# Kernel tuning notes

Hardware: AMD Instinct MI355X
Metric: run time of the kernel (lower is better)

The kernel has to match this reference:

```python
import jax, jax.numpy as jnp
import numpy as np

EMSIZE = 2048
NCLASS = 128
D1 = 2
D2 = 2
NSENT = 32768


def setup_inputs() -> dict:
    key = jax.random.key(0)
    k1, k2, k3 = jax.random.split(key, 3)
    x = jax.random.normal(k1, (NSENT, 1, EMSIZE), dtype=jnp.float32)
    # Scaled-normal params (original uses nn.init.normal_; scaling keeps tanh unsaturated)
    W1 = jax.random.normal(k2, (D1 + 1, EMSIZE, NCLASS), dtype=jnp.float32) / np.float32(np.sqrt(EMSIZE))
    b1 = jnp.zeros((1, NCLASS), dtype=jnp.float32)
    W2 = jax.random.normal(k3, (D2 + 1, NCLASS, NCLASS), dtype=jnp.float32) / np.float32(np.sqrt(NCLASS))
    b2 = jnp.zeros((1, NCLASS), dtype=jnp.float32)
    return {"structural_representations": x, "W1": W1, "b1": b1, "W2": W2, "b2": b2}


def _shift_down(y, k, n):
    # y[p] -> y[p-k], zeros for p < k (causal shift along sentence axis)
    return jnp.pad(y, ((k, 0), (0, 0)))[:n] if k > 0 else y


def reference(structural_representations, W1, b1, W2, b2):
    x = structural_representations  # [N, 1, E]
    n, _, e = x.shape
    d1 = W1.shape[0] - 1
    d2 = W2.shape[0] - 1
    c = W1.shape[-1]
    xs = x.reshape(n, e)  # [N, E]

    # Stage 1: S[p] = sum_{k=0..d1, k<=p} (x[p-k] @ W1[k] + b1)
    Y = jnp.einsum('ne,kec->knc', xs, W1)  # [d1+1, N, C]: one big GEMM per tap
    S = sum(_shift_down(Y[k], k, n) for k in range(d1 + 1))  # windowed causal sum
    pos = jnp.arange(n)
    cnt1 = (jnp.minimum(pos, d1) + 1).astype(xs.dtype)  # bias added once per valid tap
    H = jnp.tanh(S + cnt1[:, None] * b1[0])  # [N, C]

    # Stage 2 (i >= d2): Z[i] = sum_{j=0..d2} H[i-d2+j] @ W2[j] + (d2+1)*b2
    G = jnp.einsum('nc,kcd->knd', H, W2)  # [d2+1, N, C]
    Z = sum(_shift_down(G[j], d2 - j, n) for j in range(d2 + 1)) + (d2 + 1) * b2[0]

    # Fallback for i < d2: single term tanh(x[i]@W1[0]+b1) @ W2[0] + b2
    H0 = jnp.tanh(xs @ W1[0] + b1[0])
    Z0 = H0 @ W2[0] + b2[0]
    Z = jnp.where((pos >= d2)[:, None], Z, Z0)

    out = jax.nn.log_softmax(Z, axis=-1)
    return out.reshape(n, 1, c)
```

## Files before the change

### kernel.cpp

```cpp
#include <hip/hip_runtime.h>
#include <math.h>

typedef __attribute__((ext_vector_type(8))) short short8;
typedef __attribute__((ext_vector_type(4))) float f32x4;

#define MFMA16(a, b, c) __builtin_amdgcn_mfma_f32_16x16x32_bf16((a), (b), (c), 0, 0, 0)

__device__ inline void gl_lds16(const void* g, void* l) {
  __builtin_amdgcn_global_load_lds(
      (const __attribute__((address_space(1))) void*)g,
      (__attribute__((address_space(3))) void*)l, 16, 0, 0);
}

__device__ inline unsigned int pack2(float lo, float hi) {
  unsigned int ulo = __float_as_uint(lo), uhi = __float_as_uint(hi);
  return (uhi & 0xFFFF0000u) | (ulo >> 16);
}
__device__ inline unsigned short f2bf_r(float f) {
  return (unsigned short)((__float_as_uint(f) + 0x8000u) >> 16);
}
__device__ inline float bf2f(unsigned short h) {
  return __uint_as_float(((unsigned int)h) << 16);
}

__global__ __launch_bounds__(256) void k_repack_w1(const float* __restrict__ W1,
                                                   unsigned short* __restrict__ W1bt) {
  __shared__ float tile[64 * 128];
  const int b = blockIdx.x;
  const int k = b >> 5, et = b & 31;
  const int e0 = et * 64;
  const int tid = threadIdx.x;
  const float* src = W1 + (size_t)k * 262144 + (size_t)e0 * 128;
#pragma unroll
  for (int i = 0; i < 8; ++i) {
    int idx4 = tid + i * 256;
    ((f32x4*)tile)[idx4] = ((const f32x4*)src)[idx4];
  }
  __syncthreads();
#pragma unroll
  for (int i = 0; i < 4; ++i) {
    int item = tid + i * 256;
    int c = item >> 3, eo = (item & 7) * 8;
    union { unsigned short h[8]; uint4 v; } t;
#pragma unroll
    for (int u = 0; u < 8; ++u) t.h[u] = f2bf_r(tile[(eo + u) * 128 + c]);
    *(uint4*)(W1bt + (size_t)(k * 128 + c) * 2048 + e0 + eo) = t.v;
  }
}

__global__ __launch_bounds__(256) void k_repack_w2(const float* __restrict__ W2,
                                                   unsigned short* __restrict__ W2t) {
  int idx = blockIdx.x * 256 + threadIdx.x;
  int j = idx >> 14, r = idx & 16383, d = r >> 7, c = r & 127;
  W2t[idx] = f2bf_r(W2[(size_t)j * 16384 + (size_t)c * 128 + d]);
}

__global__ __launch_bounds__(256, 3) void k_gemm1(const float* __restrict__ X,
                                                  const unsigned short* __restrict__ Bt,
                                                  float* __restrict__ Y) {
  __shared__ float Alds[128 * 64];
  __shared__ unsigned short Blds[128 * 64];

  const int g = blockIdx.x;
  const int grp = g / 24, within = g % 24;
  const int cb = within >> 3, rb = grp * 8 + (within & 7);
  const int row0 = rb * 128, col0 = cb * 128;

  const int tid = threadIdx.x, wave = tid >> 6, lane = tid & 63;
  const int mrow = lane & 15, quad = lane >> 4;

  const float* agp[8];
#pragma unroll
  for (int r = 0; r < 8; ++r) {
    int row = wave * 32 + r * 4 + (lane >> 4);
    int c = (lane & 15) ^ (row & 15);
    agp[r] = X + (size_t)(row0 + row) * 2048 + c * 4;
  }
  const unsigned short* bgp[4];
#pragma unroll
  for (int r = 0; r < 4; ++r) {
    int col = wave * 32 + r * 8 + (lane >> 3);
    int c = (lane & 7) ^ (col & 7);
    bgp[r] = Bt + (size_t)(col0 + col) * 2048 + c * 8;
  }

  const int wr = (wave >> 1) * 64, wc = (wave & 1) * 64;

  f32x4 acc[4][4] = {};

  for (int k0 = 0; k0 < 2048; k0 += 64) {
#pragma unroll
    for (int r = 0; r < 8; ++r)
      gl_lds16(agp[r], (char*)Alds + (wave * 32 + r * 4) * 256);
#pragma unroll
    for (int r = 0; r < 4; ++r)
      gl_lds16(bgp[r], (char*)Blds + (wave * 32 + r * 8) * 128);
#pragma unroll
    for (int r = 0; r < 8; ++r) agp[r] += 64;
#pragma unroll
    for (int r = 0; r < 4; ++r) bgp[r] += 64;
    __syncthreads();

#pragma unroll
    for (int s = 0; s < 2; ++s) {
      short8 af[4];
#pragma unroll
      for (int rt = 0; rt < 4; ++rt) {
        int row = wr + rt * 16 + mrow;
        int c0 = s * 8 + quad * 2;
        const float* base = Alds + row * 64;
        f32x4 x0 = *(const f32x4*)(base + ((c0 ^ (row & 15)) * 4));
        f32x4 x1 = *(const f32x4*)(base + (((c0 + 1) ^ (row & 15)) * 4));
        union { unsigned int u[4]; short8 v; } t;
        t.u[0] = pack2(x0[0], x0[1]); t.u[1] = pack2(x0[2], x0[3]);
        t.u[2] = pack2(x1[0], x1[1]); t.u[3] = pack2(x1[2], x1[3]);
        af[rt] = t.v;
      }
#pragma unroll
      for (int ct = 0; ct < 4; ++ct) {
        int col = wc + ct * 16 + mrow;
        int ch = (s * 4 + quad) ^ (col & 7);
        short8 bf = *(const short8*)(Blds + col * 64 + ch * 8);
#pragma unroll
        for (int rt = 0; rt < 4; ++rt)
          acc[rt][ct] = MFMA16(af[rt], bf, acc[rt][ct]);
      }
    }
    __syncthreads();
  }

#pragma unroll
  for (int rt = 0; rt < 4; ++rt)
#pragma unroll
    for (int ct = 0; ct < 4; ++ct)
#pragma unroll
      for (int rg = 0; rg < 4; ++rg) {
        int rrow = row0 + wr + rt * 16 + quad * 4 + rg;
        int ccol = col0 + wc + ct * 16 + mrow;
        Y[(size_t)rrow * 384 + ccol] = acc[rt][ct][rg];
      }
}

#define HS 136
__global__ __launch_bounds__(256) void k_stage2(const float* __restrict__ Y,
                                                const unsigned short* __restrict__ W2t,
                                                const float* __restrict__ b1,
                                                const float* __restrict__ b2,
                                                float* __restrict__ out) {
  __shared__ unsigned short Hlds[66 * HS];
  __shared__ float zbuf[2][128];
  const int bid = blockIdx.x, tid = threadIdx.x;
  const int r0 = bid * 64;

  for (int idx = tid; idx < 66 * 128; idx += 256) {
    int hl = idx >> 7, c = idx & 127;
    int p = r0 - 2 + hl;
    float h = 0.f;
    if (p >= 0) {
      float s = Y[(size_t)p * 384 + c];
      float cnt = 1.f;
      if (p >= 1) { s += Y[(size_t)(p - 1) * 384 + 128 + c]; cnt += 1.f; }
      if (p >= 2) { s += Y[(size_t)(p - 2) * 384 + 256 + c]; cnt += 1.f; }
      h = tanhf(fmaf(cnt, b1[c], s));
    }
    Hlds[hl * HS + c] = f2bf_r(h);
  }
  __syncthreads();

  const int wave = tid >> 6, lane = tid & 63, mrow = lane & 15, quad = lane >> 4;
  f32x4 acc[8] = {};
#pragma unroll
  for (int j = 0; j < 3; ++j) {
#pragma unroll
    for (int kk = 0; kk < 4; ++kk) {
      short8 a0 = *(const short8*)&Hlds[(wave * 16 + mrow + j) * HS + kk * 32 + quad * 8];
      const unsigned short* wp = W2t + (size_t)(j * 128 + mrow) * 128 + kk * 32 + quad * 8;
#pragma unroll
      for (int ct = 0; ct < 8; ++ct)
        acc[ct] = MFMA16(a0, *(const short8*)(wp + ct * 16 * 128), acc[ct]);
    }
  }

#pragma unroll
  for (int rg = 0; rg < 4; ++rg) {
    float z[8]; float m = -1e30f;
#pragma unroll
    for (int ct = 0; ct < 8; ++ct) {
      z[ct] = acc[ct][rg] + 3.f * b2[ct * 16 + mrow];
      m = fmaxf(m, z[ct]);
    }
#pragma unroll
    for (int off = 1; off < 16; off <<= 1) m = fmaxf(m, __shfl_xor(m, off, 64));
    float s = 0.f;
#pragma unroll
    for (int ct = 0; ct < 8; ++ct) s += __expf(z[ct] - m);
#pragma unroll
    for (int off = 1; off < 16; off <<= 1) s += __shfl_xor(s, off, 64);
    float lse = m + __logf(s);
    int grow = r0 + wave * 16 + quad * 4 + rg;
    if (grow >= 2) {
      float* op = out + (size_t)grow * 128 + mrow;
#pragma unroll
      for (int ct = 0; ct < 8; ++ct) op[ct * 16] = z[ct] - lse;
    }
  }

  if (bid == 0) {
    __syncthreads();
    int row = tid >> 7, d = tid & 127;
    zbuf[row][d] = tanhf(Y[(size_t)row * 384 + d] + b1[d]);
    __syncthreads();
    float zv = b2[d];
    for (int c = 0; c < 128; ++c)
      zv = fmaf(zbuf[row][c], bf2f(W2t[(size_t)d * 128 + c]), zv);
    __syncthreads();
    zbuf[row][d] = zv;
    __syncthreads();
    float m = -1e30f;
    for (int c = 0; c < 128; ++c) m = fmaxf(m, zbuf[row][c]);
    float s = 0.f;
    for (int c = 0; c < 128; ++c) s += __expf(zbuf[row][c] - m);
    out[(size_t)row * 128 + d] = zv - m - __logf(s);
  }
}

extern "C" void kernel_launch(void* const* d_in, const int* in_sizes, int n_in,
                              void* d_out, int out_size, void* d_ws, size_t ws_size,
                              hipStream_t stream) {
  const float* X  = (const float*)d_in[0];
  const float* W1 = (const float*)d_in[1];
  const float* b1 = (const float*)d_in[2];
  const float* W2 = (const float*)d_in[3];
  const float* b2 = (const float*)d_in[4];
  float* out = (float*)d_out;

  float* Y = (float*)d_ws;
  unsigned short* W1bt = (unsigned short*)((char*)d_ws + 50331648);
  unsigned short* W2t  = (unsigned short*)((char*)d_ws + 50331648 + 1572864);

  k_repack_w1<<<96, 256, 0, stream>>>(W1, W1bt);
  k_repack_w2<<<192, 256, 0, stream>>>(W2, W2t);
  k_gemm1<<<768, 256, 0, stream>>>(X, W1bt, Y);
  k_stage2<<<512, 256, 0, stream>>>(Y, W2t, b1, b2, out);
}
```

Before: 469.2 us.

## Retile GEMM1 to 64-row blocks covering all 384 columns, store Y in bf16

GEMM1 now gives each block 64 rows of X and all 384 output columns (3 taps × 128), so each X row is read from HBM once instead of three times across column blocks. The intermediate Y is written and read as bf16 instead of fp32, halving that traffic for both kernels. In exchange there are fewer blocks (512), a larger B tile in LDS (48KB), lower occupancy (2 blocks per CU), and extra rounding error in Y before the tanh.

```diff
diff --git a/kernel.cpp b/kernel.cpp
--- a/kernel.cpp
+++ b/kernel.cpp
@@ -55,50 +55,44 @@
   W2t[idx] = f2bf_r(W2[(size_t)j * 16384 + (size_t)c * 128 + d]);
 }
 
-__global__ __launch_bounds__(256, 3) void k_gemm1(const float* __restrict__ X,
+__global__ __launch_bounds__(256, 2) void k_gemm1(const float* __restrict__ X,
                                                   const unsigned short* __restrict__ Bt,
-                                                  float* __restrict__ Y) {
-  __shared__ float Alds[128 * 64];
-  __shared__ unsigned short Blds[128 * 64];
-
-  const int g = blockIdx.x;
-  const int grp = g / 24, within = g % 24;
-  const int cb = within >> 3, rb = grp * 8 + (within & 7);
-  const int row0 = rb * 128, col0 = cb * 128;
-
+                                                  unsigned short* __restrict__ Ybf) {
+  __shared__ float Alds[64 * 64];
+  __shared__ unsigned short Blds[384 * 64];
+
+  const int r0 = blockIdx.x * 64;
   const int tid = threadIdx.x, wave = tid >> 6, lane = tid & 63;
   const int mrow = lane & 15, quad = lane >> 4;
 
-  const float* agp[8];
-#pragma unroll
-  for (int r = 0; r < 8; ++r) {
-    int row = wave * 32 + r * 4 + (lane >> 4);
+  const float* agp[4];
+#pragma unroll
+  for (int r = 0; r < 4; ++r) {
+    int row = wave * 16 + r * 4 + (lane >> 4);
     int c = (lane & 15) ^ (row & 15);
-    agp[r] = X + (size_t)(row0 + row) * 2048 + c * 4;
-  }
-  const unsigned short* bgp[4];
-#pragma unroll
-  for (int r = 0; r < 4; ++r) {
-    int col = wave * 32 + r * 8 + (lane >> 3);
+    agp[r] = X + (size_t)(r0 + row) * 2048 + c * 4;
+  }
+  const unsigned short* bgp[12];
+#pragma unroll
+  for (int r = 0; r < 12; ++r) {
+    int col = wave * 96 + r * 8 + (lane >> 3);
     int c = (lane & 7) ^ (col & 7);
-    bgp[r] = Bt + (size_t)(col0 + col) * 2048 + c * 8;
-  }
-
-  const int wr = (wave >> 1) * 64, wc = (wave & 1) * 64;
-
-  f32x4 acc[4][4] = {};
+    bgp[r] = Bt + (size_t)col * 2048 + c * 8;
+  }
+
+  f32x4 acc[4][6] = {};
 
   for (int k0 = 0; k0 < 2048; k0 += 64) {
 #pragma unroll
-    for (int r = 0; r < 8; ++r)
-      gl_lds16(agp[r], (char*)Alds + (wave * 32 + r * 4) * 256);
-#pragma unroll
     for (int r = 0; r < 4; ++r)
-      gl_lds16(bgp[r], (char*)Blds + (wave * 32 + r * 8) * 128);
-#pragma unroll
-    for (int r = 0; r < 8; ++r) agp[r] += 64;
-#pragma unroll
-    for (int r = 0; r < 4; ++r) bgp[r] += 64;
+      gl_lds16(agp[r], (char*)Alds + (wave * 16 + r * 4) * 256);
+#pragma unroll
+    for (int r = 0; r < 12; ++r)
+      gl_lds16(bgp[r], (char*)Blds + (wave * 96 + r * 8) * 128);
+#pragma unroll
+    for (int r = 0; r < 4; ++r) agp[r] += 64;
+#pragma unroll
+    for (int r = 0; r < 12; ++r) bgp[r] += 64;
     __syncthreads();
 
 #pragma unroll
@@ -106,20 +100,20 @@
       short8 af[4];
 #pragma unroll
       for (int rt = 0; rt < 4; ++rt) {
-        int row = wr + rt * 16 + mrow;
+        int row = rt * 16 + mrow;
         int c0 = s * 8 + quad * 2;
         const float* base = Alds + row * 64;
-        f32x4 x0 = *(const f32x4*)(base + ((c0 ^ (row & 15)) * 4));
-        f32x4 x1 = *(const f32x4*)(base + (((c0 + 1) ^ (row & 15)) * 4));
+        f32x4 x0 = *(const f32x4*)(base + ((c0 ^ mrow) * 4));
+        f32x4 x1 = *(const f32x4*)(base + (((c0 + 1) ^ mrow) * 4));
         union { unsigned int u[4]; short8 v; } t;
         t.u[0] = pack2(x0[0], x0[1]); t.u[1] = pack2(x0[2], x0[3]);
         t.u[2] = pack2(x1[0], x1[1]); t.u[3] = pack2(x1[2], x1[3]);
         af[rt] = t.v;
       }
 #pragma unroll
-      for (int ct = 0; ct < 4; ++ct) {
-        int col = wc + ct * 16 + mrow;
-        int ch = (s * 4 + quad) ^ (col & 7);
+      for (int ct = 0; ct < 6; ++ct) {
+        int col = wave * 96 + ct * 16 + mrow;
+        int ch = (s * 4 + quad) ^ (mrow & 7);
         short8 bf = *(const short8*)(Blds + col * 64 + ch * 8);
 #pragma unroll
         for (int rt = 0; rt < 4; ++rt)
@@ -132,17 +126,17 @@
 #pragma unroll
   for (int rt = 0; rt < 4; ++rt)
 #pragma unroll
-    for (int ct = 0; ct < 4; ++ct)
+    for (int ct = 0; ct < 6; ++ct)
 #pragma unroll
       for (int rg = 0; rg < 4; ++rg) {
-        int rrow = row0 + wr + rt * 16 + quad * 4 + rg;
-        int ccol = col0 + wc + ct * 16 + mrow;
-        Y[(size_t)rrow * 384 + ccol] = acc[rt][ct][rg];
+        int rrow = r0 + rt * 16 + quad * 4 + rg;
+        int ccol = wave * 96 + ct * 16 + mrow;
+        Ybf[(size_t)rrow * 384 + ccol] = f2bf_r(acc[rt][ct][rg]);
       }
 }
 
 #define HS 136
-__global__ __launch_bounds__(256) void k_stage2(const float* __restrict__ Y,
+__global__ __launch_bounds__(256) void k_stage2(const unsigned short* __restrict__ Yb,
                                                 const unsigned short* __restrict__ W2t,
                                                 const float* __restrict__ b1,
                                                 const float* __restrict__ b2,
@@ -157,10 +151,10 @@
     int p = r0 - 2 + hl;
     float h = 0.f;
     if (p >= 0) {
-      float s = Y[(size_t)p * 384 + c];
+      float s = bf2f(Yb[(size_t)p * 384 + c]);
       float cnt = 1.f;
-      if (p >= 1) { s += Y[(size_t)(p - 1) * 384 + 128 + c]; cnt += 1.f; }
-      if (p >= 2) { s += Y[(size_t)(p - 2) * 384 + 256 + c]; cnt += 1.f; }
+      if (p >= 1) { s += bf2f(Yb[(size_t)(p - 1) * 384 + 128 + c]); cnt += 1.f; }
+      if (p >= 2) { s += bf2f(Yb[(size_t)(p - 2) * 384 + 256 + c]); cnt += 1.f; }
       h = tanhf(fmaf(cnt, b1[c], s));
     }
     Hlds[hl * HS + c] = f2bf_r(h);
@@ -208,7 +202,7 @@
   if (bid == 0) {
     __syncthreads();
     int row = tid >> 7, d = tid & 127;
-    zbuf[row][d] = tanhf(Y[(size_t)row * 384 + d] + b1[d]);
+    zbuf[row][d] = tanhf(bf2f(Yb[(size_t)row * 384 + d]) + b1[d]);
     __syncthreads();
     float zv = b2[d];
     for (int c = 0; c < 128; ++c)
@@ -234,12 +228,12 @@
   const float* b2 = (const float*)d_in[4];
   float* out = (float*)d_out;
 
-  float* Y = (float*)d_ws;
-  unsigned short* W1bt = (unsigned short*)((char*)d_ws + 50331648);
-  unsigned short* W2t  = (unsigned short*)((char*)d_ws + 50331648 + 1572864);
+  unsigned short* Ybf  = (unsigned short*)d_ws;
+  unsigned short* W1bt = (unsigned short*)((char*)d_ws + 25165824);
+  unsigned short* W2t  = (unsigned short*)((char*)d_ws + 25165824 + 1572864);
 
   k_repack_w1<<<96, 256, 0, stream>>>(W1, W1bt);
   k_repack_w2<<<192, 256, 0, stream>>>(W2, W2t);
-  k_gemm1<<<768, 256, 0, stream>>>(X, W1bt, Y);
-  k_stage2<<<512, 256, 0, stream>>>(Y, W2t, b1, b2, out);
-}
+  k_gemm1<<<512, 256, 0, stream>>>(X, W1bt, Ybf);
+  k_stage2<<<512, 256, 0, stream>>>(Ybf, W2t, b1, b2, out);
+}
```

Measured after the change: 460.5 us. About the same (-1.9%).
